# Performance work log

Hardware: AMD Instinct MI355X
Metric: run time of the kernel (lower is better)

The kernel has to match this reference:

```python
import jax, jax.numpy as jnp
import numpy as np

B, S, H = 256, 512, 256  # batch, seq_len, input_size == hidden_size (forced by h_shape logic)


def setup_inputs() -> dict:
    key = jax.random.key(0)
    ks = jax.random.split(key, 8)
    scale = 1.0 / np.sqrt(H)

    def w(k, shape):
        return jax.random.normal(k, shape, dtype=jnp.float32) * scale

    # x last feature channel doubles as the (nonnegative) time-delta signal
    x = jax.random.uniform(ks[0], (B, S, H), dtype=jnp.float32)
    return dict(
        x=x,
        Wx0=w(ks[1], (H, 4 * H)), Wh0=w(ks[2], (H, 4 * H)), b0=jnp.zeros((4 * H,), jnp.float32),
        Wd0=w(ks[3], (H, H)), bd0=jnp.zeros((H,), jnp.float32),
        Wx1=w(ks[4], (H, 4 * H)), Wh1=w(ks[5], (H, 4 * H)), b1=jnp.zeros((4 * H,), jnp.float32),
        Wd1=w(ks[6], (H, H)), bd1=jnp.zeros((H,), jnp.float32),
    )


def _tlstm_layer(x, Wx, Wh, b, Wd, bd):
    """One T-LSTM layer over a full sequence. x: [B, S, F] -> ([B, S, H], hT, cT)."""
    # Precompute input projections for all timesteps (hoisted out of the recurrence)
    xg = jnp.einsum('bsf,fg->bsg', x, Wx) + b          # [B, S, 4H]
    dt = x[..., -1:]                                    # time delta channel [B, S, 1]
    decay = 1.0 / jnp.log(jnp.e + dt)                   # 'log' time-decay g(dt)

    h0 = jnp.zeros((x.shape[0], Wh.shape[0]), x.dtype)
    c0 = jnp.zeros_like(h0)

    def step(carry, inp):
        h, c = carry
        xg_t, dec_t = inp
        # T-LSTM memory decomposition: decay short-term component of cell state
        cs = jnp.tanh(c @ Wd + bd)                      # short-term memory C_S
        c_adj = c - cs + cs * dec_t                     # C_T + C_S * g(dt)
        g = xg_t + h @ Wh                               # fused gate pre-activations [B, 4H]
        i, f, o, cand = jnp.split(g, 4, axis=-1)
        c_new = jax.nn.sigmoid(f) * c_adj + jax.nn.sigmoid(i) * jnp.tanh(cand)
        h_new = jax.nn.sigmoid(o) * jnp.tanh(c_new)
        return (h_new, c_new), h_new

    (hT, cT), hs = jax.lax.scan(
        step, (h0, c0), (jnp.swapaxes(xg, 0, 1), jnp.swapaxes(decay, 0, 1)))
    return jnp.swapaxes(hs, 0, 1), hT, cT               # [B, S, H], [B, H], [B, H]


def reference(x, Wx0, Wh0, b0, Wd0, bd0, Wx1, Wh1, b1, Wd1, bd1):
    y0, h0, c0 = _tlstm_layer(x, Wx0, Wh0, b0, Wd0, bd0)
    y1, h1, c1 = _tlstm_layer(y0, Wx1, Wh1, b1, Wd1, bd1)
    # matches (layer_output, last_state_list) of the torch module, flattened
    return (y1, h0, c0, h1, c1)
```

## Files before the change

### kernel.cpp

```cpp
#include <hip/hip_runtime.h>
#include <stdint.h>

#define B_ 256
#define S_ 512
#define H_ 256
#define G_ 1024
#define CHUNK 32
#define NCHUNK (S_ / CHUNK)

typedef __attribute__((ext_vector_type(8))) short bf16x8;
typedef __attribute__((ext_vector_type(4))) float f32x4;

__device__ __forceinline__ unsigned short f2bf(float f) {
    unsigned u = __builtin_bit_cast(unsigned, f);
    unsigned r = u + 0x7fffu + ((u >> 16) & 1u);
    return (unsigned short)(r >> 16);
}
__device__ __forceinline__ float bf2f(unsigned short v) {
    return __builtin_bit_cast(float, (unsigned)v << 16);
}
__device__ __forceinline__ float bfbits_lo(unsigned v) {
    return __builtin_bit_cast(float, (unsigned)(v << 16));
}
__device__ __forceinline__ float bfbits_hi(unsigned v) {
    return __builtin_bit_cast(float, v & 0xffff0000u);
}
__device__ __forceinline__ float sigmoidf_(float x) { return 1.f / (1.f + __expf(-x)); }
__device__ __forceinline__ float tanhf_(float x) { return 2.f / (1.f + __expf(-2.f * x)) - 1.f; }

__global__ void prep_w(const float* __restrict__ W, unsigned short* __restrict__ Wp, int NT) {
    int tid = blockIdx.x * 256 + threadIdx.x;
    int total = NT * 8 * 64;
    if (tid >= total) return;
    int l = tid & 63, kk = (tid >> 6) & 7, nt = tid >> 9;
    int n = nt * 16 + (l & 15);
    int k0 = kk * 32 + (l >> 4) * 8;
    int N = NT * 16;
    unsigned short v[8];
#pragma unroll
    for (int i = 0; i < 8; i++) v[i] = f2bf(W[(size_t)(k0 + i) * N + n]);
    uint4 o;
    o.x = (unsigned)v[0] | ((unsigned)v[1] << 16);
    o.y = (unsigned)v[2] | ((unsigned)v[3] << 16);
    o.z = (unsigned)v[4] | ((unsigned)v[5] << 16);
    o.w = (unsigned)v[6] | ((unsigned)v[7] << 16);
    *(uint4*)(Wp + (size_t)tid * 8) = o;
}

__global__ void prep_decay(const float* __restrict__ x, float* __restrict__ dec, int n) {
    int i = blockIdx.x * 256 + threadIdx.x;
    if (i < n) dec[i] = 1.f / __logf(2.718281828459045f + x[(size_t)i * H_ + (H_ - 1)]);
}

template <bool SRCF32>
__device__ void gemm_body(const void* __restrict__ src, const unsigned short* __restrict__ Wp,
                          const float* __restrict__ bias, unsigned short* __restrict__ xgp,
                          int chunk, short* Albs) {
    const int tid = threadIdx.x;
    const int bx = blockIdx.x;
    const int by = blockIdx.y;
    const int r0 = bx * 128;
    const int t_loc = r0 >> 8;
    const int b0 = r0 & 255;
    const int sg = chunk * CHUNK + t_loc;
    {
        const int m = tid >> 1, kh = tid & 1;
        const size_t rowbase = ((size_t)(b0 + m) * S_ + sg) * H_ + kh * 128;
        if constexpr (SRCF32) {
            const float* p = (const float*)src + rowbase;
#pragma unroll
            for (int jo = 0; jo < 16; jo++) {
                int k = kh * 128 + jo * 8;
                float4 a = *(const float4*)(p + jo * 8);
                float4 b = *(const float4*)(p + jo * 8 + 4);
                int slot = ((m >> 4) * 8 + (k >> 5)) * 64 + ((m & 15) | (((k >> 3) & 3) << 4));
                uint4 o;
                o.x = (unsigned)f2bf(a.x) | ((unsigned)f2bf(a.y) << 16);
                o.y = (unsigned)f2bf(a.z) | ((unsigned)f2bf(a.w) << 16);
                o.z = (unsigned)f2bf(b.x) | ((unsigned)f2bf(b.y) << 16);
                o.w = (unsigned)f2bf(b.z) | ((unsigned)f2bf(b.w) << 16);
                *(uint4*)&Albs[slot * 8] = o;
            }
        } else {
            const unsigned short* p = (const unsigned short*)src + rowbase;
#pragma unroll
            for (int jo = 0; jo < 16; jo++) {
                int k = kh * 128 + jo * 8;
                uint4 o = *(const uint4*)(p + jo * 8);
                int slot = ((m >> 4) * 8 + (k >> 5)) * 64 + ((m & 15) | (((k >> 3) & 3) << 4));
                *(uint4*)&Albs[slot * 8] = o;
            }
        }
    }
    __syncthreads();
    const int w = tid >> 6, l = tid & 63;
    const int wm = w >> 1, wn = w & 1;
    const int col = l & 15;
    float bv[4];
#pragma unroll
    for (int q = 0; q < 4; q++) bv[q] = bias[(by * 8 + wn * 4 + q) * 16 + col];
    f32x4 acc[4][4];
#pragma unroll
    for (int mi = 0; mi < 4; mi++)
#pragma unroll
        for (int q = 0; q < 4; q++) {
            acc[mi][q][0] = bv[q]; acc[mi][q][1] = bv[q];
            acc[mi][q][2] = bv[q]; acc[mi][q][3] = bv[q];
        }
    const bf16x8* Wp8 = (const bf16x8*)Wp;
#pragma unroll
    for (int kk = 0; kk < 8; kk++) {
        bf16x8 af[4], bfr[4];
#pragma unroll
        for (int mi = 0; mi < 4; mi++)
            af[mi] = *(const bf16x8*)&Albs[(((wm * 4 + mi) * 8 + kk) * 64 + l) * 8];
#pragma unroll
        for (int q = 0; q < 4; q++)
            bfr[q] = Wp8[((size_t)(by * 8 + wn * 4 + q) * 8 + kk) * 64 + l];
#pragma unroll
        for (int mi = 0; mi < 4; mi++)
#pragma unroll
            for (int q = 0; q < 4; q++)
                acc[mi][q] = __builtin_amdgcn_mfma_f32_16x16x32_bf16(af[mi], bfr[q], acc[mi][q], 0, 0, 0);
    }
    const int rblk0 = r0 >> 4;
#pragma unroll
    for (int mi = 0; mi < 4; mi++) {
        int rowblk = rblk0 + wm * 4 + mi;
#pragma unroll
        for (int q = 0; q < 4; q++) {
            int qg = by * 8 + wn * 4 + q;
            uint2 o;
            o.x = (unsigned)f2bf(acc[mi][q][0]) | ((unsigned)f2bf(acc[mi][q][1]) << 16);
            o.y = (unsigned)f2bf(acc[mi][q][2]) | ((unsigned)f2bf(acc[mi][q][3]) << 16);
            *(uint2*)&xgp[(((size_t)rowblk * 64 + qg) * 64 + l) * 4] = o;
        }
    }
}

__global__ __launch_bounds__(256) void gemm_dual(const float* __restrict__ x,
                                                 const unsigned short* __restrict__ y0bf,
                                                 const unsigned short* __restrict__ Wp0,
                                                 const float* __restrict__ bias0,
                                                 const unsigned short* __restrict__ Wp1,
                                                 const float* __restrict__ bias1,
                                                 unsigned short* __restrict__ xgpA,
                                                 unsigned short* __restrict__ xgpB, int c0, int c1) {
    extern __shared__ short Albs[];
    if (blockIdx.z == 0) {
        if (c0 < 0) return;
        gemm_body<true>(x, Wp0, bias0, xgpA, c0, Albs);
    } else {
        if (c1 < 0) return;
        gemm_body<false>(y0bf, Wp1, bias1, xgpB, c1, Albs);
    }
}

template <bool ISL0>
__device__ void rec_run(const unsigned short* __restrict__ xgp, const bf16x8* __restrict__ Whp8,
                        const bf16x8* __restrict__ Wdp8, const float* __restrict__ bd,
                        const float* __restrict__ dec_in, void* __restrict__ yout,
                        float* __restrict__ dec_out, unsigned short* __restrict__ h_state,
                        float* __restrict__ c_state, int chunk, int bblk, char* smem) {
    short* hb = (short*)smem;
    short* cb = (short*)(smem + 8192);
    const int tid = threadIdx.x;
    const int w = tid >> 6, l = tid & 63;
    const int lgrp = l >> 4, col = l & 15;
    const int b0 = bblk * 16;
    const int n = w * 16 + col;
    const float bdv = bd[n];

    float creg[4];
    if (chunk == 0) {
#pragma unroll
        for (int r = 0; r < 4; r++) creg[r] = 0.f;
        for (int i = tid; i < 4096; i += 1024) { hb[i] = 0; cb[i] = 0; }
    } else {
#pragma unroll
        for (int i = 0; i < 4; i++) {
            int idx = tid + i * 1024;
            int row = idx >> 8, nn = idx & 255;
            int sw = nn ^ ((row & 7) << 3);
            hb[row * 256 + sw] = (short)h_state[(size_t)(b0 + row) * H_ + nn];
            cb[row * 256 + sw] = (short)f2bf(c_state[(size_t)(b0 + row) * H_ + nn]);
        }
#pragma unroll
        for (int r = 0; r < 4; r++)
            creg[r] = c_state[(size_t)(b0 + lgrp * 4 + r) * H_ + n];
    }
    const uint2* xg8 = (const uint2*)xgp;
    uint2 xc[4], xn[4];
#pragma unroll
    for (int q = 0; q < 4; q++)
        xc[q] = xg8[((size_t)bblk * 64 + (q * 16 + w)) * 64 + l];
    float dn[4];
#pragma unroll
    for (int r = 0; r < 4; r++)
        dn[r] = dec_in[(size_t)(b0 + lgrp * 4 + r) * S_ + chunk * CHUNK];
    __syncthreads();

    bf16x8 wfb[2][4], wdb[2];
#pragma unroll
    for (int q = 0; q < 4; q++) wfb[0][q] = Whp8[((size_t)(q * 16 + w) * 8 + 0) * 64 + l];
    wdb[0] = Wdp8[((size_t)w * 8 + 0) * 64 + l];

#pragma unroll 1
    for (int t = 0; t < CHUNK; ++t) {
        const int tg = chunk * CHUNK + t;
        unsigned tz = 0;
        asm volatile("" : "+v"(tz));
        const int lz = l + (int)tz;
        float dcur[4];
#pragma unroll
        for (int r = 0; r < 4; r++) dcur[r] = dn[r];
        f32x4 csacc = {0.f, 0.f, 0.f, 0.f};
        f32x4 gacc[4];
#pragma unroll
        for (int q = 0; q < 4; q++) {
            uint2 v = xc[q];
            gacc[q][0] = bfbits_lo(v.x);
            gacc[q][1] = bfbits_hi(v.x);
            gacc[q][2] = bfbits_lo(v.y);
            gacc[q][3] = bfbits_hi(v.y);
        }
#pragma unroll
        for (int kk = 0; kk < 8; kk++) {
            const int cur = kk & 1, nb = cur ^ 1;
            const int kn = (kk + 1) & 7;
#pragma unroll
            for (int q = 0; q < 4; q++)
                wfb[nb][q] = Whp8[((size_t)(q * 16 + w) * 8 + kn) * 64 + lz];
            wdb[nb] = Wdp8[((size_t)w * 8 + kn) * 64 + lz];
            const int ha = col * 256 + ((kk * 32 + lgrp * 8) ^ ((col & 7) << 3));
            bf16x8 hf = *(const bf16x8*)&hb[ha];
            bf16x8 cf = *(const bf16x8*)&cb[ha];
            csacc = __builtin_amdgcn_mfma_f32_16x16x32_bf16(cf, wdb[cur], csacc, 0, 0, 0);
#pragma unroll
            for (int q = 0; q < 4; q++)
                gacc[q] = __builtin_amdgcn_mfma_f32_16x16x32_bf16(hf, wfb[cur][q], gacc[q], 0, 0, 0);
        }
        __builtin_amdgcn_sched_barrier(0);
        __builtin_amdgcn_s_barrier();
        __builtin_amdgcn_sched_barrier(0);
        const int tn = (t + 1 < CHUNK) ? t + 1 : t;
        {
            int rb = tn * 16 + bblk;
#pragma unroll
            for (int q = 0; q < 4; q++)
                xn[q] = xg8[((size_t)rb * 64 + (q * 16 + w)) * 64 + l];
            int tgn = chunk * CHUNK + tn;
#pragma unroll
            for (int r = 0; r < 4; r++)
                dn[r] = dec_in[(size_t)(b0 + lgrp * 4 + r) * S_ + tgn];
        }
#pragma unroll
        for (int r = 0; r < 4; r++) {
            int row = lgrp * 4 + r;
            float cs = tanhf_(csacc[r] + bdv);
            float cadj = creg[r] - cs + cs * dcur[r];
            float iv = sigmoidf_(gacc[0][r]);
            float fv = sigmoidf_(gacc[1][r]);
            float ov = sigmoidf_(gacc[2][r]);
            float cd = tanhf_(gacc[3][r]);
            float cn = fv * cadj + iv * cd;
            float hn = ov * tanhf_(cn);
            creg[r] = cn;
            int sw = n ^ ((row & 7) << 3);
            unsigned short hnb = f2bf(hn);
            hb[row * 256 + sw] = (short)hnb;
            cb[row * 256 + sw] = (short)f2bf(cn);
            size_t yi = ((size_t)(b0 + row) * S_ + tg) * H_ + n;
            if constexpr (ISL0) {
                ((unsigned short*)yout)[yi] = hnb;
                if (w == 15 && col == 15)
                    dec_out[(size_t)(b0 + row) * S_ + tg] = 1.f / __logf(2.718281828459045f + hn);
            } else {
                ((float*)yout)[yi] = hn;
            }
            if (t == CHUNK - 1) {
                h_state[(size_t)(b0 + row) * H_ + n] = hnb;
                c_state[(size_t)(b0 + row) * H_ + n] = cn;
            }
        }
        asm volatile("s_waitcnt lgkmcnt(0)" ::: "memory");
        __builtin_amdgcn_s_barrier();
        __builtin_amdgcn_sched_barrier(0);
#pragma unroll
        for (int q = 0; q < 4; q++) xc[q] = xn[q];
    }
}

__global__ __launch_bounds__(1024, 4) void rec_fused(
    const unsigned short* __restrict__ xgpA, const unsigned short* __restrict__ Whp0,
    const unsigned short* __restrict__ Wdp0, const float* __restrict__ bd0,
    const float* __restrict__ dec0, unsigned short* __restrict__ y0bf,
    float* __restrict__ dec1, unsigned short* __restrict__ hs0, float* __restrict__ cs0,
    const unsigned short* __restrict__ xgpB, const unsigned short* __restrict__ Whp1,
    const unsigned short* __restrict__ Wdp1, const float* __restrict__ bd1,
    float* __restrict__ y1, unsigned short* __restrict__ hs1, float* __restrict__ cs1,
    int c0, int c1) {
    extern __shared__ char smem[];
    int lay = blockIdx.x >> 4, bblk = blockIdx.x & 15;
    if (lay == 0) {
        if (c0 < 0) return;
        rec_run<true>(xgpA, (const bf16x8*)Whp0, (const bf16x8*)Wdp0, bd0, dec0, y0bf, dec1,
                      hs0, cs0, c0, bblk, smem);
    } else {
        if (c1 < 0) return;
        rec_run<false>(xgpB, (const bf16x8*)Whp1, (const bf16x8*)Wdp1, bd1, dec1, y1, nullptr,
                       hs1, cs1, c1, bblk, smem);
    }
}

__global__ void copy_tail(const unsigned short* __restrict__ h0, const float* __restrict__ c0,
                          const unsigned short* __restrict__ h1, const float* __restrict__ c1,
                          float* __restrict__ out) {
    int i = blockIdx.x * 256 + threadIdx.x;
    if (i >= 4 * 65536) return;
    int which = i >> 16, j = i & 65535;
    float v = which == 0 ? bf2f(h0[j]) : which == 1 ? c0[j] : which == 2 ? bf2f(h1[j]) : c1[j];
    out[i] = v;
}

extern "C" void kernel_launch(void* const* d_in, const int* in_sizes, int n_in, void* d_out,
                              int out_size, void* d_ws, size_t ws_size, hipStream_t stream) {
    (void)in_sizes; (void)n_in; (void)out_size; (void)ws_size;
    const float* x   = (const float*)d_in[0];
    const float* Wx0 = (const float*)d_in[1];
    const float* Wh0 = (const float*)d_in[2];
    const float* b0  = (const float*)d_in[3];
    const float* Wd0 = (const float*)d_in[4];
    const float* bd0 = (const float*)d_in[5];
    const float* Wx1 = (const float*)d_in[6];
    const float* Wh1 = (const float*)d_in[7];
    const float* b1  = (const float*)d_in[8];
    const float* Wd1 = (const float*)d_in[9];
    const float* bd1 = (const float*)d_in[10];

    char* ws = (char*)d_ws;
    size_t off = 0;
    auto take = [&](size_t bytes) { void* p = ws + off; off += (bytes + 255) & ~(size_t)255; return p; };
    unsigned short* wxp0 = (unsigned short*)take(524288);
    unsigned short* whp0 = (unsigned short*)take(524288);
    unsigned short* wdp0 = (unsigned short*)take(131072);
    unsigned short* wxp1 = (unsigned short*)take(524288);
    unsigned short* whp1 = (unsigned short*)take(524288);
    unsigned short* wdp1 = (unsigned short*)take(131072);
    float* dec0 = (float*)take(524288);
    float* dec1 = (float*)take(524288);
    unsigned short* hs0 = (unsigned short*)take(131072);
    float* cs0 = (float*)take(262144);
    unsigned short* hs1 = (unsigned short*)take(131072);
    float* cs1 = (float*)take(262144);
    unsigned short* y0bf = (unsigned short*)take(67108864);
    unsigned short* xgpA = (unsigned short*)take(16777216);
    unsigned short* xgpB = (unsigned short*)take(16777216);

    const size_t smem_rec = 16384;
    (void)hipFuncSetAttribute(reinterpret_cast<const void*>(&rec_fused),
                              hipFuncAttributeMaxDynamicSharedMemorySize, (int)smem_rec);
    (void)hipFuncSetAttribute(reinterpret_cast<const void*>(&gemm_dual),
                              hipFuncAttributeMaxDynamicSharedMemorySize, 65536);

    prep_w<<<128, 256, 0, stream>>>(Wx0, wxp0, 64);
    prep_w<<<128, 256, 0, stream>>>(Wh0, whp0, 64);
    prep_w<<<32, 256, 0, stream>>>(Wd0, wdp0, 16);
    prep_w<<<128, 256, 0, stream>>>(Wx1, wxp1, 64);
    prep_w<<<128, 256, 0, stream>>>(Wh1, whp1, 64);
    prep_w<<<32, 256, 0, stream>>>(Wd1, wdp1, 16);
    prep_decay<<<512, 256, 0, stream>>>(x, dec0, B_ * S_);

    float* y1 = (float*)d_out;
    for (int s = 0; s <= NCHUNK; ++s) {
        int c0 = (s < NCHUNK) ? s : -1;
        int c1 = (s >= 1) ? s - 1 : -1;
        gemm_dual<<<dim3(64, 8, 2), 256, 65536, stream>>>(x, y0bf, wxp0, b0, wxp1, b1,
                                                          xgpA, xgpB, c0, c1);
        rec_fused<<<32, 1024, smem_rec, stream>>>(xgpA, whp0, wdp0, bd0, dec0, y0bf, dec1,
                                                  hs0, cs0, xgpB, whp1, wdp1, bd1, y1,
                                                  hs1, cs1, c0, c1);
    }
    copy_tail<<<1024, 256, 0, stream>>>(hs0, cs0, hs1, cs1, y1 + (size_t)B_ * S_ * H_);
}
```

Before: 4.889 ms.

## Double-buffer h/c state in LDS to drop a per-step barrier; keep Wd in registers

```diff
diff --git a/kernel.cpp b/kernel.cpp
--- a/kernel.cpp
+++ b/kernel.cpp
@@ -162,8 +162,6 @@
                         const float* __restrict__ dec_in, void* __restrict__ yout,
                         float* __restrict__ dec_out, unsigned short* __restrict__ h_state,
                         float* __restrict__ c_state, int chunk, int bblk, char* smem) {
-    short* hb = (short*)smem;
-    short* cb = (short*)(smem + 8192);
     const int tid = threadIdx.x;
     const int w = tid >> 6, l = tid & 63;
     const int lgrp = l >> 4, col = l & 15;
@@ -171,23 +169,31 @@
     const int n = w * 16 + col;
     const float bdv = bd[n];
 
+    bf16x8 wd[8];
+#pragma unroll
+    for (int kk = 0; kk < 8; kk++) wd[kk] = Wdp8[((size_t)w * 8 + kk) * 64 + l];
+
     float creg[4];
-    if (chunk == 0) {
-#pragma unroll
-        for (int r = 0; r < 4; r++) creg[r] = 0.f;
-        for (int i = tid; i < 4096; i += 1024) { hb[i] = 0; cb[i] = 0; }
-    } else {
-#pragma unroll
-        for (int i = 0; i < 4; i++) {
-            int idx = tid + i * 1024;
-            int row = idx >> 8, nn = idx & 255;
-            int sw = nn ^ ((row & 7) << 3);
-            hb[row * 256 + sw] = (short)h_state[(size_t)(b0 + row) * H_ + nn];
-            cb[row * 256 + sw] = (short)f2bf(c_state[(size_t)(b0 + row) * H_ + nn]);
-        }
-#pragma unroll
-        for (int r = 0; r < 4; r++)
-            creg[r] = c_state[(size_t)(b0 + lgrp * 4 + r) * H_ + n];
+    {
+        short* hb0 = (short*)smem;
+        short* cb0 = (short*)(smem + 8192);
+        if (chunk == 0) {
+#pragma unroll
+            for (int r = 0; r < 4; r++) creg[r] = 0.f;
+            for (int i = tid; i < 4096; i += 1024) { hb0[i] = 0; cb0[i] = 0; }
+        } else {
+#pragma unroll
+            for (int i = 0; i < 4; i++) {
+                int idx = tid + i * 1024;
+                int row = idx >> 8, nn = idx & 255;
+                int sw = nn ^ ((row & 7) << 3);
+                hb0[row * 256 + sw] = (short)h_state[(size_t)(b0 + row) * H_ + nn];
+                cb0[row * 256 + sw] = (short)f2bf(c_state[(size_t)(b0 + row) * H_ + nn]);
+            }
+#pragma unroll
+            for (int r = 0; r < 4; r++)
+                creg[r] = c_state[(size_t)(b0 + lgrp * 4 + r) * H_ + n];
+        }
     }
     const uint2* xg8 = (const uint2*)xgp;
     uint2 xc[4], xn[4];
@@ -200,17 +206,24 @@
         dn[r] = dec_in[(size_t)(b0 + lgrp * 4 + r) * S_ + chunk * CHUNK];
     __syncthreads();
 
-    bf16x8 wfb[2][4], wdb[2];
+    bf16x8 wfb[2][4];
 #pragma unroll
     for (int q = 0; q < 4; q++) wfb[0][q] = Whp8[((size_t)(q * 16 + w) * 8 + 0) * 64 + l];
-    wdb[0] = Wdp8[((size_t)w * 8 + 0) * 64 + l];
 
 #pragma unroll 1
     for (int t = 0; t < CHUNK; ++t) {
         const int tg = chunk * CHUNK + t;
-        unsigned tz = 0;
-        asm volatile("" : "+v"(tz));
-        const int lz = l + (int)tz;
+        const int par = t & 1;
+        const short* hb = (const short*)(smem + par * 16384);
+        const short* cb = (const short*)(smem + par * 16384 + 8192);
+        short* hx = (short*)(smem + (par ^ 1) * 16384);
+        short* cx = (short*)(smem + (par ^ 1) * 16384 + 8192);
+        const bf16x8* WhpT;
+        {
+            unsigned long long tz = 0;
+            asm volatile("" : "+s"(tz));
+            WhpT = (const bf16x8*)((const char*)Whp8 + tz);
+        }
         float dcur[4];
 #pragma unroll
         for (int r = 0; r < 4; r++) dcur[r] = dn[r];
@@ -230,19 +243,15 @@
             const int kn = (kk + 1) & 7;
 #pragma unroll
             for (int q = 0; q < 4; q++)
-                wfb[nb][q] = Whp8[((size_t)(q * 16 + w) * 8 + kn) * 64 + lz];
-            wdb[nb] = Wdp8[((size_t)w * 8 + kn) * 64 + lz];
+                wfb[nb][q] = WhpT[((size_t)(q * 16 + w) * 8 + kn) * 64 + l];
             const int ha = col * 256 + ((kk * 32 + lgrp * 8) ^ ((col & 7) << 3));
             bf16x8 hf = *(const bf16x8*)&hb[ha];
             bf16x8 cf = *(const bf16x8*)&cb[ha];
-            csacc = __builtin_amdgcn_mfma_f32_16x16x32_bf16(cf, wdb[cur], csacc, 0, 0, 0);
+            csacc = __builtin_amdgcn_mfma_f32_16x16x32_bf16(cf, wd[kk], csacc, 0, 0, 0);
 #pragma unroll
             for (int q = 0; q < 4; q++)
                 gacc[q] = __builtin_amdgcn_mfma_f32_16x16x32_bf16(hf, wfb[cur][q], gacc[q], 0, 0, 0);
         }
-        __builtin_amdgcn_sched_barrier(0);
-        __builtin_amdgcn_s_barrier();
-        __builtin_amdgcn_sched_barrier(0);
         const int tn = (t + 1 < CHUNK) ? t + 1 : t;
         {
             int rb = tn * 16 + bblk;
@@ -268,8 +277,8 @@
             creg[r] = cn;
             int sw = n ^ ((row & 7) << 3);
             unsigned short hnb = f2bf(hn);
-            hb[row * 256 + sw] = (short)hnb;
-            cb[row * 256 + sw] = (short)f2bf(cn);
+            hx[row * 256 + sw] = (short)hnb;
+            cx[row * 256 + sw] = (short)f2bf(cn);
             size_t yi = ((size_t)(b0 + row) * S_ + tg) * H_ + n;
             if constexpr (ISL0) {
                 ((unsigned short*)yout)[yi] = hnb;
@@ -357,7 +366,7 @@
     unsigned short* xgpA = (unsigned short*)take(16777216);
     unsigned short* xgpB = (unsigned short*)take(16777216);
 
-    const size_t smem_rec = 16384;
+    const size_t smem_rec = 32768;
     (void)hipFuncSetAttribute(reinterpret_cast<const void*>(&rec_fused),
                               hipFuncAttributeMaxDynamicSharedMemorySize, (int)smem_rec);
     (void)hipFuncSetAttribute(reinterpret_cast<const void*>(&gemm_dual),
```

Measured after the change: 4.864 ms. Within noise of the previous version (-0.5%).
